# Kernel optimization log

Hardware: AMD Instinct MI355X
Metric: run time of the kernel (lower is better)

The kernel has to match this reference:

```python
import jax, jax.numpy as jnp
import numpy as np

NUM_TIMESCALES = 16
MAX_TIME = 100.0
N_HEADS = 4
MLP_WIDTH = 128
HIDDEN_EACH = 128  # hidden_size // attn_n_heads = 512 // 4


def setup_inputs() -> dict:
    key = jax.random.key(0)
    ks = jax.random.split(key, 8)
    B, ROWS_PER_PAT, V = 32, 64, 32
    R = B * ROWS_PER_PAT
    # patient i has counts[i] observations, laid out row-major in its block of rows
    counts = 512 + 16 * np.arange(B)
    M = np.zeros((R, V), np.int32)
    for i in range(B):
        flat = M[i * ROWS_PER_PAT:(i + 1) * ROWS_PER_PAT].reshape(-1)
        flat[:counts[i]] = 1
    n_obs = int(counts.sum())        # 24320
    max_n_obs = int(counts.max())    # 1008
    n_in = 2 * NUM_TIMESCALES + 2    # 34

    def lin(k, o, i_):
        kw, kb = jax.random.split(k)
        return (jax.random.normal(kw, (o, i_)) * (1.0 / np.sqrt(i_)),
                jax.random.normal(kb, (o,)) * 0.01)

    W0, b0 = lin(ks[0], MLP_WIDTH, n_in)
    W1, b1 = lin(ks[1], MLP_WIDTH, MLP_WIDTH)
    W2, b2 = lin(ks[2], HIDDEN_EACH, MLP_WIDTH)
    Wq, bq = lin(ks[3], HIDDEN_EACH, HIDDEN_EACH)
    Wk, bk = lin(ks[4], HIDDEN_EACH, HIDDEN_EACH)
    return {
        "times": jax.random.uniform(ks[5], (R,)) * MAX_TIME,
        "time_ptr": jnp.arange(R + 1),
        "X": jax.random.normal(ks[6], (R, V)),
        "M": jnp.asarray(M),
        "obs_idx": jnp.repeat(jnp.arange(B), ROWS_PER_PAT),
        "pat_idx": jnp.arange(B),
        "W0": W0, "b0": b0, "W1": W1, "b1": b1, "W2": W2, "b2": b2,
        "Wq": Wq, "bq": bq, "Wk": Wk, "bk": bk,
        "n_obs": n_obs, "max_n_obs": max_n_obs,
    }


def reference(times, time_ptr, X, M, obs_idx, pat_idx,
              W0, b0, W1, b1, W2, b2, Wq, bq, Wk, bk, n_obs, max_n_obs):
    B = pat_idx.shape[0]
    # --- ragged scatter: (time_row, var) observations -> padded per-patient sets ---
    rows, cols = jnp.nonzero(M, size=n_obs)          # row-major, grouped by patient
    p = obs_idx[rows]                                # patient id per observation
    vals = X[rows, cols]
    t_arr = jnp.repeat(times, jnp.diff(time_ptr), total_repeat_length=X.shape[0])
    t = t_arr[rows]
    lens = jnp.bincount(p, length=B)
    starts = jnp.cumsum(lens) - lens
    pos = jnp.arange(n_obs) - starts[p]              # within-patient slot index
    Sv = jnp.zeros((B, max_n_obs), X.dtype).at[p, pos].set(cols.astype(X.dtype))
    Sx = jnp.zeros((B, max_n_obs), X.dtype).at[p, pos].set(vals)
    St = jnp.zeros((B, max_n_obs), X.dtype).at[p, pos].set(t)
    pad = jnp.arange(max_n_obs)[None, :] >= lens[:, None]   # True = padding
    # --- time embedding + feature concat: [sin, cos, var, value] ---
    timescales = MAX_TIME ** jnp.linspace(0.0, 1.0, NUM_TIMESCALES)
    st = St[..., None] / timescales
    new_X = jnp.concatenate([jnp.sin(st), jnp.cos(st), Sv[..., None], Sx[..., None]], axis=-1)
    # --- encoder MLP (depth 3 -> 1 hidden layer, eval mode: dropout is identity) ---
    h = jax.nn.relu(new_X @ W0.T + b0)
    h = jax.nn.relu(h @ W1.T + b1)
    enc = h @ W2.T + b2                              # [B, L, 128]
    # --- masked self-attention weights (only q/k matter; output is discarded) ---
    L = max_n_obs
    hd = HIDDEN_EACH // N_HEADS
    q = (enc @ Wq.T + bq).reshape(B, L, N_HEADS, hd)
    k = (enc @ Wk.T + bk).reshape(B, L, N_HEADS, hd)
    scores = jnp.einsum('blhd,bmhd->bhlm', q, k) / np.sqrt(hd)
    scores = jnp.where(pad[:, None, None, :], -1e30, scores)
    attn = jax.nn.softmax(scores, axis=-1)           # [B, H, L, L]
    w = attn[:, :, -1, :]                            # last-query attention row
    summed = jnp.einsum('bhl,ble->bhe', w, enc)      # [B, H, 128]
    return summed.reshape(B, -1)                     # [B, 512]
```

## Files before the change

kernel.cpp:

```cpp
#include <hip/hip_runtime.h>

#define B_PAT 32
#define RTOT 2048
#define NV 32
#define LMAX 1008
#define NTS 16
#define NIN 64
#define TLD 72
#define HW 128
#define LDSP 136
#define NCH2 32
#define ELD 132
#define RLD 136

typedef __attribute__((ext_vector_type(8))) short short8;
typedef __attribute__((ext_vector_type(4))) float floatx4;

__device__ __forceinline__ ushort f2b(float f) {
  unsigned int x = __float_as_uint(f);
  unsigned int r = (x + 0x7FFFu + ((x >> 16) & 1u)) >> 16;
  return (ushort)r;
}
__device__ __forceinline__ unsigned int pack2(ushort lo, ushort hi) {
  return (unsigned int)lo | ((unsigned int)hi << 16);
}
__device__ __forceinline__ float tscale(int i) {
  return exp2f((float)i * (6.643856189774724f / 15.0f));
}

__global__ __launch_bounds__(256) void kA(
    const float* __restrict__ times, const int* __restrict__ time_ptr,
    const int* __restrict__ M, const float* __restrict__ W0,
    const float* __restrict__ W1, const float* __restrict__ W2,
    int* __restrict__ row_cnt, float* __restrict__ trow,
    ushort* __restrict__ W0p, ushort* __restrict__ W1b, ushort* __restrict__ W2b)
{
  const int blk = blockIdx.x, t = threadIdx.x;
  if (blk >= 8) {
    if (blk == 8) {
      for (int i = t; i < HW * NIN; i += 256) {
        int n = i >> 6, k = i & 63;
        W0p[i] = (k < 34) ? f2b(W0[n * 34 + k]) : (ushort)0;
      }
    } else if (blk == 9) {
      for (int i = t; i < HW * HW; i += 256) W1b[i] = f2b(W1[i]);
    } else {
      for (int i = t; i < HW * HW; i += 256) W2b[i] = f2b(W2[i]);
    }
    return;
  }
  const int r = blk * 256 + t;
  const int4* mp = (const int4*)(M + r * NV);
  int c = 0;
#pragma unroll
  for (int q = 0; q < 8; ++q) {
    int4 m4 = mp[q];
    c += (m4.x != 0) + (m4.y != 0) + (m4.z != 0) + (m4.w != 0);
  }
  row_cnt[r] = c;
  int lo = 0, hi = RTOT - 1;
  while (lo < hi) { int mid = (lo + hi + 1) >> 1; if (time_ptr[mid] <= r) lo = mid; else hi = mid - 1; }
  trow[r] = times[lo];
}

__global__ __launch_bounds__(256) void kB(
    const int* __restrict__ obs_idx, const int* __restrict__ row_cnt,
    int* __restrict__ base, int* __restrict__ rowstart, int* __restrict__ lens)
{
  const int t = threadIdx.x;
  const int lane = t & 63, wv = t >> 6;
  __shared__ int wsum[4];
  __shared__ int gpre[RTOT + 1];
  __shared__ int rowstart_s[B_PAT + 1];
  int cnt[8], pref[8];
  int a = 0;
  const int rbase = t * 8;
#pragma unroll
  for (int j = 0; j < 8; ++j) {
    cnt[j] = row_cnt[rbase + j];
    pref[j] = a; a += cnt[j];
  }
  int incl = a;
  for (int off = 1; off < 64; off <<= 1) {
    int v = __shfl_up(incl, off);
    if (lane >= off) incl += v;
  }
  if (lane == 63) wsum[wv] = incl;
  if (t == 0) rowstart_s[B_PAT] = RTOT;
  __syncthreads();
  int wbase = 0;
  for (int w = 0; w < wv; ++w) wbase += wsum[w];
  int excl = wbase + incl - a;
#pragma unroll
  for (int j = 0; j < 8; ++j) gpre[rbase + j] = excl + pref[j];
  if (t == 255) gpre[RTOT] = excl + a;
  for (int r = t; r < RTOT; r += 256) {
    int b = obs_idx[r];
    if (r == 0 || obs_idx[r - 1] != b) rowstart_s[b] = r;
  }
  __syncthreads();
  if (t < B_PAT) {
    int rs = rowstart_s[t], re = rowstart_s[t + 1];
    lens[t] = gpre[re] - gpre[rs];
    rowstart[t] = rs;
  }
  if (t == 0) rowstart[B_PAT] = RTOT;
  for (int r = t; r < RTOT; r += 256)
    base[r] = gpre[r] - gpre[rowstart_s[obs_idx[r]]];
}

__global__ __launch_bounds__(256) void kC(
    const int* __restrict__ M, const float* __restrict__ X,
    const float* __restrict__ trow, const int* __restrict__ base,
    const int* __restrict__ row_cnt, const int* __restrict__ rowstart,
    const int* __restrict__ lens,
    const float* __restrict__ W0, const float* __restrict__ b0,
    const float* __restrict__ W1, const float* __restrict__ b1,
    const float* __restrict__ W2, const float* __restrict__ b2,
    const float* __restrict__ Wq, const float* __restrict__ bq,
    const float* __restrict__ Wk, float* __restrict__ r_all)
{
  const int b = blockIdx.x;
  const int t = threadIdx.x;
  __shared__ float x_s[64];
  __shared__ float h0[HW], h1[HW], eq[HW], q_s[HW], part[256];
  __shared__ int rc_s[2];
  if (t < 64) x_s[t] = 0.0f;
  if (t == 0) {
    const int pos = LMAX - 1;
    if (pos < lens[b]) {
      int r = rowstart[b];
      while (base[r] + row_cnt[r] <= pos) ++r;
      int k = pos - base[r], c = 0;
      for (int cc = 0; cc < NV; ++cc)
        if (M[r * NV + cc] != 0) { if (k == 0) { c = cc; break; } --k; }
      rc_s[0] = r; rc_s[1] = c;
    } else rc_s[0] = -1;
  }
  __syncthreads();
  if (rc_s[0] < 0) {
    if (t >= 16 && t < 32) x_s[t] = 1.0f;
  } else {
    int r = rc_s[0], c = rc_s[1];
    if (t < 16) {
      float a = trow[r] / tscale(t);
      x_s[t] = sinf(a); x_s[16 + t] = cosf(a);
    }
    if (t == 0) { x_s[32] = (float)c; x_s[33] = X[r * NV + c]; }
  }
  __syncthreads();
  if (t < HW) {
    float a = b0[t];
#pragma unroll 2
    for (int k = 0; k < 34; ++k) a += W0[t * 34 + k] * x_s[k];
    h0[t] = fmaxf(a, 0.0f);
  }
  __syncthreads();
  {
    int oo = t & 127, hf = t >> 7;
    float a = 0.f;
    const float* wr = W1 + oo * HW + hf * 64;
#pragma unroll 8
    for (int k = 0; k < 64; ++k) a += wr[k] * h0[hf * 64 + k];
    part[t] = a;
  }
  __syncthreads();
  if (t < HW) h1[t] = fmaxf(part[t] + part[t + 128] + b1[t], 0.0f);
  __syncthreads();
  {
    int oo = t & 127, hf = t >> 7;
    float a = 0.f;
    const float* wr = W2 + oo * HW + hf * 64;
#pragma unroll 8
    for (int k = 0; k < 64; ++k) a += wr[k] * h1[hf * 64 + k];
    part[t] = a;
  }
  __syncthreads();
  if (t < HW) eq[t] = part[t] + part[t + 128] + b2[t];
  __syncthreads();
  {
    int oo = t & 127, hf = t >> 7;
    float a = 0.f;
    const float* wr = Wq + oo * HW + hf * 64;
#pragma unroll 8
    for (int k = 0; k < 64; ++k) a += wr[k] * eq[hf * 64 + k];
    part[t] = a;
  }
  __syncthreads();
  if (t < HW) q_s[t] = part[t] + part[t + 128] + bq[t];
  __syncthreads();
  const float scale = 0.17677669529663687f;
  for (int idx = t; idx < 512; idx += 256) {
    int h = idx >> 7, e = idx & 127;
    float a = 0.f;
#pragma unroll 8
    for (int d = 0; d < 32; ++d) a += Wk[(h * 32 + d) * HW + e] * q_s[h * 32 + d];
    r_all[b * 512 + idx] = a * scale;
  }
}

__global__ __launch_bounds__(256) void kD(
    const int* __restrict__ M, const float* __restrict__ X,
    const float* __restrict__ trow, const int* __restrict__ base,
    const int* __restrict__ row_cnt, const int* __restrict__ rowstart,
    const ushort* __restrict__ W0p, const float* __restrict__ b0,
    const ushort* __restrict__ W1b, const float* __restrict__ b1,
    const ushort* __restrict__ W2b, const float* __restrict__ b2,
    const float* __restrict__ r_all, float* __restrict__ partial,
    float2* __restrict__ mxsm)
{
  const int bx = blockIdx.x;
  const int b = bx >> 5, j = bx & 31;
  const int t = threadIdx.x;
  const int wv = t >> 6, lane = t & 63;
  const int rs = rowstart[b], re = rowstart[b + 1];
  const int r0 = rs + 2 * j;
  if (r0 >= re) {
    if (t < 4) mxsm[bx * 4 + t] = make_float2(-1e30f, 0.0f);
    return;
  }
  const int r1 = r0 + 1;
  const bool has1 = (r1 < re);
  const int pstart = base[r0];
  const int valid = row_cnt[r0] + (has1 ? row_cnt[r1] : 0);
  if (valid <= 0) {
    if (t < 4) mxsm[bx * 4 + t] = make_float2(-1e30f, 0.0f);
    return;
  }
  __shared__ __align__(16) char arena[55296];
  ushort* tile = (ushort*)(arena);
  ushort* bufA = (ushort*)(arena + 9216);
  float*  encs = (float*)(arena);
  ushort* bufB = (ushort*)(arena + 33792);
  float*  r_s  = (float*)(arena + 51200);
  float*  lg   = (float*)(arena + 53376);
  unsigned int* mapP = (unsigned int*)(arena + 54400);
  unsigned int* mapT = (unsigned int*)(arena + 54656);
  ushort* tps  = (ushort*)(arena + 54912);
  float*  mx_s = (float*)(arena + 55040);
  float*  sm_s = (float*)(arena + 55056);
  {
    uint4 z = make_uint4(0u, 0u, 0u, 0u);
    uint4* tp = (uint4*)tile;
    for (int i = t; i < 576; i += 256) tp[i] = z;
    for (int i = t; i < 512; i += 256)
      r_s[(i >> 7) * RLD + (i & 127)] = r_all[b * 512 + i];
  }
  __syncthreads();
  if (wv == 0) {
    int rr = lane >> 5, cc = lane & 31;
    int r = r0 + rr;
    bool present = (rr == 0 || has1) ? (M[r * NV + cc] != 0) : false;
    unsigned long long mask = __ballot(present);
    unsigned int mh = (rr == 0) ? (unsigned int)mask : (unsigned int)(mask >> 32);
    if (present) {
      int rank = __popc(mh & ((1u << cc) - 1u));
      int lp = base[r] - pstart + rank;
      mapP[lp] = pack2(f2b((float)cc), f2b(X[r * NV + cc]));
      mapT[lp] = (unsigned int)rr;
    }
  }
  if (wv == 1 && lane < 32) {
    int rr = lane >> 4, i = lane & 15;
    if (rr == 0 || has1) {
      float a = trow[r0 + rr] / tscale(i);
      tps[rr * 32 + i] = f2b(sinf(a));
      tps[rr * 32 + 16 + i] = f2b(cosf(a));
    }
  }
  __syncthreads();
  {
    int lp = t >> 2, jj = t & 3;
    if (lp < valid) {
      int rr = (int)mapT[lp];
      unsigned int* dst = (unsigned int*)(tile + lp * TLD);
      const unsigned int* tp = ((const unsigned int*)tps) + rr * 16;
      if (jj == 0) {
#pragma unroll
        for (int k = 0; k < 8; ++k) dst[k] = tp[k];
      } else if (jj == 1) {
#pragma unroll
        for (int k = 0; k < 8; ++k) dst[8 + k] = tp[8 + k];
      } else if (jj == 2) {
        dst[16] = mapP[lp];
      }
    }
  }
  __syncthreads();
  const int m16 = lane & 15, quad = lane >> 4;
  const int rowl = wv * 16 + m16;
  {
    const short8* ar = (const short8*)(tile + rowl * TLD);
    short8 a0 = ar[quad];
    short8 a1 = ar[4 + quad];
#pragma unroll
    for (int nt = 0; nt < 8; ++nt) {
      int n = nt * 16 + m16;
      const short8* br = (const short8*)(W0p + n * NIN);
      floatx4 acc = {0.f, 0.f, 0.f, 0.f};
      acc = __builtin_amdgcn_mfma_f32_16x16x32_bf16(a0, br[quad], acc, 0, 0, 0);
      acc = __builtin_amdgcn_mfma_f32_16x16x32_bf16(a1, br[4 + quad], acc, 0, 0, 0);
      float bias = b0[n];
#pragma unroll
      for (int i = 0; i < 4; ++i) {
        float vv = fmaxf(acc[i] + bias, 0.0f);
        bufA[(wv * 16 + quad * 4 + i) * LDSP + n] = f2b(vv);
      }
    }
  }
  __syncthreads();
  {
#pragma unroll
    for (int nt = 0; nt < 8; ++nt) {
      int n = nt * 16 + m16;
      floatx4 acc = {0.f, 0.f, 0.f, 0.f};
#pragma unroll
      for (int ks = 0; ks < 4; ++ks) {
        short8 a = *(const short8*)(bufA + rowl * LDSP + ks * 32 + quad * 8);
        short8 bb = *(const short8*)(W1b + n * HW + ks * 32 + quad * 8);
        acc = __builtin_amdgcn_mfma_f32_16x16x32_bf16(a, bb, acc, 0, 0, 0);
      }
      float bias = b1[n];
#pragma unroll
      for (int i = 0; i < 4; ++i) {
        float vv = fmaxf(acc[i] + bias, 0.0f);
        bufB[(wv * 16 + quad * 4 + i) * LDSP + n] = f2b(vv);
      }
    }
  }
  __syncthreads();
  {
#pragma unroll
    for (int nt = 0; nt < 8; ++nt) {
      int n = nt * 16 + m16;
      floatx4 acc = {0.f, 0.f, 0.f, 0.f};
#pragma unroll
      for (int ks = 0; ks < 4; ++ks) {
        short8 a = *(const short8*)(bufB + rowl * LDSP + ks * 32 + quad * 8);
        short8 bb = *(const short8*)(W2b + n * HW + ks * 32 + quad * 8);
        acc = __builtin_amdgcn_mfma_f32_16x16x32_bf16(a, bb, acc, 0, 0, 0);
      }
      float bias = b2[n];
#pragma unroll
      for (int i = 0; i < 4; ++i)
        encs[(wv * 16 + quad * 4 + i) * ELD + n] = acc[i] + bias;
    }
  }
  __syncthreads();
  {
    int m = t >> 2, h = t & 3;
    if (m < valid) {
      const float4* ev = (const float4*)(&encs[m * ELD]);
      const float4* rv = (const float4*)(&r_s[h * RLD]);
      float acc = 0.f;
#pragma unroll
      for (int e4 = 0; e4 < 32; ++e4) {
        float4 v = ev[e4], r = rv[e4];
        acc += v.x * r.x + v.y * r.y + v.z * r.z + v.w * r.w;
      }
      lg[h * 64 + m] = acc;
    }
  }
  __syncthreads();
  {
    float v = (lane < valid) ? lg[wv * 64 + lane] : -1e30f;
    float mx = v;
#pragma unroll
    for (int o = 32; o >= 1; o >>= 1) mx = fmaxf(mx, __shfl_xor(mx, o));
    float p = (lane < valid) ? expf(v - mx) : 0.f;
    lg[wv * 64 + lane] = p;
    float sm = p;
#pragma unroll
    for (int o = 32; o >= 1; o >>= 1) sm += __shfl_xor(sm, o);
    if (lane == 0) { mx_s[wv] = mx; sm_s[wv] = sm; }
  }
  __syncthreads();
  for (int idx = t; idx < 512; idx += 256) {
    int h = idx >> 7, e = idx & 127;
    float acc = 0.f;
    for (int m = 0; m < valid; ++m)
      acc += lg[h * 64 + m] * encs[m * ELD + e];
    partial[(size_t)bx * 512 + idx] = acc;
  }
  if (t < 4) mxsm[bx * 4 + t] = make_float2(mx_s[t], sm_s[t]);
}

__global__ __launch_bounds__(256) void k4_combine(
    const float* __restrict__ partial, const float2* __restrict__ mxsm,
    float* __restrict__ out)
{
  const int b = blockIdx.x;
  const int tid = threadIdx.x;
  __shared__ float f_s[NCH2 * 4];
  if (tid < 4) {
    int h = tid;
    float2 v[NCH2];
    float M = -1e30f;
#pragma unroll
    for (int c = 0; c < NCH2; ++c) {
      v[c] = mxsm[(b * NCH2 + c) * 4 + h];
      if (v[c].y > 0.f) M = fmaxf(M, v[c].x);
    }
    float S = 0.f;
#pragma unroll
    for (int c = 0; c < NCH2; ++c)
      if (v[c].y > 0.f) S += v[c].y * expf(v[c].x - M);
    float invS = 1.0f / S;
#pragma unroll
    for (int c = 0; c < NCH2; ++c)
      f_s[c * 4 + h] = (v[c].y > 0.f) ? expf(v[c].x - M) * invS : 0.f;
  }
  __syncthreads();
  for (int idx = tid; idx < 512; idx += 256) {
    int h = idx >> 7;
    float acc = 0.f;
#pragma unroll
    for (int c = 0; c < NCH2; ++c)
      acc += partial[((size_t)(b * NCH2 + c)) * 512 + idx] * f_s[c * 4 + h];
    out[b * 512 + idx] = acc;
  }
}

extern "C" void kernel_launch(void* const* d_in, const int* in_sizes, int n_in,
                              void* d_out, int out_size, void* d_ws, size_t ws_size,
                              hipStream_t stream) {
  const float* times = (const float*)d_in[0];
  const int* time_ptr = (const int*)d_in[1];
  const float* X = (const float*)d_in[2];
  const int* M = (const int*)d_in[3];
  const int* obs_idx = (const int*)d_in[4];
  const float* W0 = (const float*)d_in[6];
  const float* b0 = (const float*)d_in[7];
  const float* W1 = (const float*)d_in[8];
  const float* b1 = (const float*)d_in[9];
  const float* W2 = (const float*)d_in[10];
  const float* b2 = (const float*)d_in[11];
  const float* Wq = (const float*)d_in[12];
  const float* bq = (const float*)d_in[13];
  const float* Wk = (const float*)d_in[14];
  float* out = (float*)d_out;

  char* ws = (char*)d_ws;
  size_t off = 0;
  int* row_cnt = (int*)(ws + off); off += RTOT * 4;
  float* trow = (float*)(ws + off); off += RTOT * 4;
  int* base = (int*)(ws + off); off += RTOT * 4;
  int* rowstart = (int*)(ws + off); off += 256;
  int* lens = (int*)(ws + off); off += 256;
  ushort* W0p = (ushort*)(ws + off); off += (size_t)HW * NIN * 2;
  ushort* W1b = (ushort*)(ws + off); off += (size_t)HW * HW * 2;
  ushort* W2b = (ushort*)(ws + off); off += (size_t)HW * HW * 2;
  float* r_all = (float*)(ws + off); off += (size_t)B_PAT * 512 * 4;
  float* partial = (float*)(ws + off); off += (size_t)B_PAT * NCH2 * 512 * 4;
  float2* mxsm = (float2*)(ws + off); off += (size_t)B_PAT * NCH2 * 4 * 8;

  kA<<<11, 256, 0, stream>>>(times, time_ptr, M, W0, W1, W2, row_cnt, trow, W0p, W1b, W2b);
  kB<<<1, 256, 0, stream>>>(obs_idx, row_cnt, base, rowstart, lens);
  kC<<<B_PAT, 256, 0, stream>>>(M, X, trow, base, row_cnt, rowstart, lens,
                                W0, b0, W1, b1, W2, b2, Wq, bq, Wk, r_all);
  kD<<<B_PAT * NCH2, 256, 0, stream>>>(M, X, trow, base, row_cnt, rowstart,
                                       W0p, b0, W1b, b1, W2b, b2, r_all, partial, mxsm);
  k4_combine<<<B_PAT, 256, 0, stream>>>(partial, mxsm, out);
}
```

Measured before the change: 167.2 us.

## Fuse preprocessing kernels into per-patient prep and rechunk encoder by observation count

```diff
diff --git a/kernel.cpp b/kernel.cpp
--- a/kernel.cpp
+++ b/kernel.cpp
@@ -9,7 +9,8 @@
 #define TLD 72
 #define HW 128
 #define LDSP 136
-#define NCH2 32
+#define NCH 16
+#define CH 63
 #define ELD 132
 #define RLD 136
 
@@ -28,125 +29,102 @@
   return exp2f((float)i * (6.643856189774724f / 15.0f));
 }
 
-__global__ __launch_bounds__(256) void kA(
+__global__ __launch_bounds__(256) void kP(
     const float* __restrict__ times, const int* __restrict__ time_ptr,
-    const int* __restrict__ M, const float* __restrict__ W0,
-    const float* __restrict__ W1, const float* __restrict__ W2,
-    int* __restrict__ row_cnt, float* __restrict__ trow,
-    ushort* __restrict__ W0p, ushort* __restrict__ W1b, ushort* __restrict__ W2b)
-{
-  const int blk = blockIdx.x, t = threadIdx.x;
-  if (blk >= 8) {
-    if (blk == 8) {
-      for (int i = t; i < HW * NIN; i += 256) {
-        int n = i >> 6, k = i & 63;
-        W0p[i] = (k < 34) ? f2b(W0[n * 34 + k]) : (ushort)0;
-      }
-    } else if (blk == 9) {
-      for (int i = t; i < HW * HW; i += 256) W1b[i] = f2b(W1[i]);
-    } else {
-      for (int i = t; i < HW * HW; i += 256) W2b[i] = f2b(W2[i]);
-    }
-    return;
-  }
-  const int r = blk * 256 + t;
-  const int4* mp = (const int4*)(M + r * NV);
-  int c = 0;
-#pragma unroll
-  for (int q = 0; q < 8; ++q) {
-    int4 m4 = mp[q];
-    c += (m4.x != 0) + (m4.y != 0) + (m4.z != 0) + (m4.w != 0);
-  }
-  row_cnt[r] = c;
-  int lo = 0, hi = RTOT - 1;
-  while (lo < hi) { int mid = (lo + hi + 1) >> 1; if (time_ptr[mid] <= r) lo = mid; else hi = mid - 1; }
-  trow[r] = times[lo];
-}
-
-__global__ __launch_bounds__(256) void kB(
-    const int* __restrict__ obs_idx, const int* __restrict__ row_cnt,
-    int* __restrict__ base, int* __restrict__ rowstart, int* __restrict__ lens)
-{
-  const int t = threadIdx.x;
-  const int lane = t & 63, wv = t >> 6;
-  __shared__ int wsum[4];
-  __shared__ int gpre[RTOT + 1];
-  __shared__ int rowstart_s[B_PAT + 1];
-  int cnt[8], pref[8];
-  int a = 0;
-  const int rbase = t * 8;
-#pragma unroll
-  for (int j = 0; j < 8; ++j) {
-    cnt[j] = row_cnt[rbase + j];
-    pref[j] = a; a += cnt[j];
-  }
-  int incl = a;
-  for (int off = 1; off < 64; off <<= 1) {
-    int v = __shfl_up(incl, off);
-    if (lane >= off) incl += v;
-  }
-  if (lane == 63) wsum[wv] = incl;
-  if (t == 0) rowstart_s[B_PAT] = RTOT;
-  __syncthreads();
-  int wbase = 0;
-  for (int w = 0; w < wv; ++w) wbase += wsum[w];
-  int excl = wbase + incl - a;
-#pragma unroll
-  for (int j = 0; j < 8; ++j) gpre[rbase + j] = excl + pref[j];
-  if (t == 255) gpre[RTOT] = excl + a;
-  for (int r = t; r < RTOT; r += 256) {
-    int b = obs_idx[r];
-    if (r == 0 || obs_idx[r - 1] != b) rowstart_s[b] = r;
-  }
-  __syncthreads();
-  if (t < B_PAT) {
-    int rs = rowstart_s[t], re = rowstart_s[t + 1];
-    lens[t] = gpre[re] - gpre[rs];
-    rowstart[t] = rs;
-  }
-  if (t == 0) rowstart[B_PAT] = RTOT;
-  for (int r = t; r < RTOT; r += 256)
-    base[r] = gpre[r] - gpre[rowstart_s[obs_idx[r]]];
-}
-
-__global__ __launch_bounds__(256) void kC(
-    const int* __restrict__ M, const float* __restrict__ X,
-    const float* __restrict__ trow, const int* __restrict__ base,
-    const int* __restrict__ row_cnt, const int* __restrict__ rowstart,
-    const int* __restrict__ lens,
+    const float* __restrict__ X, const int* __restrict__ M,
+    const int* __restrict__ obs_idx,
     const float* __restrict__ W0, const float* __restrict__ b0,
     const float* __restrict__ W1, const float* __restrict__ b1,
     const float* __restrict__ W2, const float* __restrict__ b2,
     const float* __restrict__ Wq, const float* __restrict__ bq,
-    const float* __restrict__ Wk, float* __restrict__ r_all)
+    const float* __restrict__ Wk,
+    int* __restrict__ pbase_g, int* __restrict__ rowstart_g,
+    int* __restrict__ lens, float* __restrict__ trow_g,
+    ushort* __restrict__ W0p, ushort* __restrict__ W1b, ushort* __restrict__ W2b,
+    float* __restrict__ r_all)
 {
   const int b = blockIdx.x;
   const int t = threadIdx.x;
+  if (b >= B_PAT) {
+    if (b == B_PAT) {
+      for (int i = t; i < HW * NIN; i += 256) {
+        int n = i >> 6, k = i & 63;
+        W0p[i] = (k < 34) ? f2b(W0[n * 34 + k]) : (ushort)0;
+      }
+    } else if (b == B_PAT + 1) {
+      for (int i = t; i < HW * HW; i += 256) W1b[i] = f2b(W1[i]);
+    } else {
+      for (int i = t; i < HW * HW; i += 256) W2b[i] = f2b(W2[i]);
+    }
+    return;
+  }
+  __shared__ int rs_s, re_s;
+  __shared__ int cnt_s[64];
+  __shared__ int pbase_s[65];
+  __shared__ float tval_s[64];
+  __shared__ int qrc[3];
   __shared__ float x_s[64];
   __shared__ float h0[HW], h1[HW], eq[HW], q_s[HW], part[256];
-  __shared__ int rc_s[2];
+  for (int r = t * 8; r < t * 8 + 8; ++r) {
+    if (obs_idx[r] == b) {
+      if (r == 0 || obs_idx[r - 1] != b) rs_s = r;
+      if (r == RTOT - 1 || obs_idx[r + 1] != b) re_s = r + 1;
+    }
+  }
+  __syncthreads();
+  const int rs = rs_s, re = re_s;
+  const int n = re - rs;
+  if (t < 64) {
+    int c = 0;
+    if (t < n) {
+      const int4* mp = (const int4*)(M + (size_t)(rs + t) * NV);
+#pragma unroll
+      for (int q = 0; q < 8; ++q) {
+        int4 m4 = mp[q];
+        c += (m4.x != 0) + (m4.y != 0) + (m4.z != 0) + (m4.w != 0);
+      }
+      int lo = 0, hi = RTOT - 1, r = rs + t;
+      while (lo < hi) { int mid = (lo + hi + 1) >> 1; if (time_ptr[mid] <= r) lo = mid; else hi = mid - 1; }
+      tval_s[t] = times[lo];
+      trow_g[r] = times[lo];
+    }
+    cnt_s[t] = c;
+  }
+  __syncthreads();
+  if (t < 64) {
+    int incl = cnt_s[t];
+    for (int off = 1; off < 64; off <<= 1) {
+      int v = __shfl_up(incl, off);
+      if (t >= off) incl += v;
+    }
+    pbase_s[t + 1] = incl;
+    if (t == 0) pbase_s[0] = 0;
+  }
+  __syncthreads();
+  const int len = pbase_s[64];
+  if (t < 65) pbase_g[b * 65 + t] = pbase_s[t];
+  if (t == 0) { rowstart_g[b] = rs; lens[b] = len; }
+  if (t == 0) {
+    if (LMAX - 1 < len) {
+      int lr = 0;
+      while (pbase_s[lr + 1] <= LMAX - 1) ++lr;
+      int k = (LMAX - 1) - pbase_s[lr], col = 0;
+      for (int cc = 0; cc < NV; ++cc)
+        if (M[(size_t)(rs + lr) * NV + cc] != 0) { if (k == 0) { col = cc; break; } --k; }
+      qrc[0] = lr; qrc[1] = col; qrc[2] = 1;
+    } else qrc[2] = 0;
+  }
   if (t < 64) x_s[t] = 0.0f;
-  if (t == 0) {
-    const int pos = LMAX - 1;
-    if (pos < lens[b]) {
-      int r = rowstart[b];
-      while (base[r] + row_cnt[r] <= pos) ++r;
-      int k = pos - base[r], c = 0;
-      for (int cc = 0; cc < NV; ++cc)
-        if (M[r * NV + cc] != 0) { if (k == 0) { c = cc; break; } --k; }
-      rc_s[0] = r; rc_s[1] = c;
-    } else rc_s[0] = -1;
-  }
-  __syncthreads();
-  if (rc_s[0] < 0) {
+  __syncthreads();
+  if (qrc[2] == 0) {
     if (t >= 16 && t < 32) x_s[t] = 1.0f;
   } else {
-    int r = rc_s[0], c = rc_s[1];
+    int lr = qrc[0], col = qrc[1];
     if (t < 16) {
-      float a = trow[r] / tscale(t);
+      float a = tval_s[lr] / tscale(t);
       x_s[t] = sinf(a); x_s[16 + t] = cosf(a);
     }
-    if (t == 0) { x_s[32] = (float)c; x_s[33] = X[r * NV + c]; }
+    if (t == 0) { x_s[32] = (float)col; x_s[33] = X[(size_t)(rs + lr) * NV + col]; }
   }
   __syncthreads();
   if (t < HW) {
@@ -199,10 +177,10 @@
   }
 }
 
-__global__ __launch_bounds__(256) void kD(
+__global__ __launch_bounds__(256) void kF(
     const int* __restrict__ M, const float* __restrict__ X,
-    const float* __restrict__ trow, const int* __restrict__ base,
-    const int* __restrict__ row_cnt, const int* __restrict__ rowstart,
+    const int* __restrict__ pbase_g, const int* __restrict__ rowstart_g,
+    const int* __restrict__ lens, const float* __restrict__ trow_g,
     const ushort* __restrict__ W0p, const float* __restrict__ b0,
     const ushort* __restrict__ W1b, const float* __restrict__ b1,
     const ushort* __restrict__ W2b, const float* __restrict__ b2,
@@ -210,83 +188,76 @@
     float2* __restrict__ mxsm)
 {
   const int bx = blockIdx.x;
-  const int b = bx >> 5, j = bx & 31;
+  const int b = bx >> 4, c = bx & 15;
   const int t = threadIdx.x;
-  const int wv = t >> 6, lane = t & 63;
-  const int rs = rowstart[b], re = rowstart[b + 1];
-  const int r0 = rs + 2 * j;
-  if (r0 >= re) {
-    if (t < 4) mxsm[bx * 4 + t] = make_float2(-1e30f, 0.0f);
-    return;
-  }
-  const int r1 = r0 + 1;
-  const bool has1 = (r1 < re);
-  const int pstart = base[r0];
-  const int valid = row_cnt[r0] + (has1 ? row_cnt[r1] : 0);
+  const int len = lens[b];
+  const int start = c * CH;
+  int valid = len - start; if (valid > CH) valid = CH;
   if (valid <= 0) {
     if (t < 4) mxsm[bx * 4 + t] = make_float2(-1e30f, 0.0f);
     return;
   }
-  __shared__ __align__(16) char arena[55296];
-  ushort* tile = (ushort*)(arena);
-  ushort* bufA = (ushort*)(arena + 9216);
-  float*  encs = (float*)(arena);
-  ushort* bufB = (ushort*)(arena + 33792);
-  float*  r_s  = (float*)(arena + 51200);
-  float*  lg   = (float*)(arena + 53376);
-  unsigned int* mapP = (unsigned int*)(arena + 54400);
-  unsigned int* mapT = (unsigned int*)(arena + 54656);
-  ushort* tps  = (ushort*)(arena + 54912);
-  float*  mx_s = (float*)(arena + 55040);
-  float*  sm_s = (float*)(arena + 55056);
+  __shared__ ushort tile[64 * TLD];
+  __shared__ ushort bufA[64 * LDSP];
+  __shared__ ushort bufB[64 * LDSP];
+  __shared__ float encs[64 * ELD];
+  __shared__ float r_s[4 * RLD];
+  __shared__ float lg[4 * 64];
+  __shared__ unsigned int umask[64];
+  __shared__ float tval[64];
+  __shared__ int pbase_s[65];
+  __shared__ float inv_ts[NTS];
+  __shared__ float mx_s[4], sm_s[4];
+  const int rs = rowstart_g[b];
   {
     uint4 z = make_uint4(0u, 0u, 0u, 0u);
     uint4* tp = (uint4*)tile;
-    for (int i = t; i < 576; i += 256) tp[i] = z;
+    for (int i = t; i < 64 * TLD / 8; i += 256) tp[i] = z;
     for (int i = t; i < 512; i += 256)
       r_s[(i >> 7) * RLD + (i & 127)] = r_all[b * 512 + i];
   }
-  __syncthreads();
-  if (wv == 0) {
-    int rr = lane >> 5, cc = lane & 31;
-    int r = r0 + rr;
-    bool present = (rr == 0 || has1) ? (M[r * NV + cc] != 0) : false;
-    unsigned long long mask = __ballot(present);
-    unsigned int mh = (rr == 0) ? (unsigned int)mask : (unsigned int)(mask >> 32);
-    if (present) {
-      int rank = __popc(mh & ((1u << cc) - 1u));
-      int lp = base[r] - pstart + rank;
-      mapP[lp] = pack2(f2b((float)cc), f2b(X[r * NV + cc]));
-      mapT[lp] = (unsigned int)rr;
-    }
-  }
-  if (wv == 1 && lane < 32) {
-    int rr = lane >> 4, i = lane & 15;
-    if (rr == 0 || has1) {
-      float a = trow[r0 + rr] / tscale(i);
-      tps[rr * 32 + i] = f2b(sinf(a));
-      tps[rr * 32 + 16 + i] = f2b(cosf(a));
-    }
-  }
-  __syncthreads();
-  {
-    int lp = t >> 2, jj = t & 3;
-    if (lp < valid) {
-      int rr = (int)mapT[lp];
-      unsigned int* dst = (unsigned int*)(tile + lp * TLD);
-      const unsigned int* tp = ((const unsigned int*)tps) + rr * 16;
-      if (jj == 0) {
-#pragma unroll
-        for (int k = 0; k < 8; ++k) dst[k] = tp[k];
-      } else if (jj == 1) {
-#pragma unroll
-        for (int k = 0; k < 8; ++k) dst[8 + k] = tp[8 + k];
-      } else if (jj == 2) {
-        dst[16] = mapP[lp];
-      }
-    }
-  }
-  __syncthreads();
+  if (t < 64) {
+    int r = rs + t;
+    unsigned int mk = 0;
+    const int* mp = M + (size_t)r * NV;
+#pragma unroll
+    for (int cc = 0; cc < NV; ++cc) mk |= (mp[cc] != 0 ? 1u : 0u) << cc;
+    umask[t] = mk;
+    tval[t] = trow_g[r];
+  } else if (t < 129) {
+    pbase_s[t - 64] = pbase_g[b * 65 + (t - 64)];
+  } else if (t >= 136 && t < 136 + NTS) {
+    inv_ts[t - 136] = 1.0f / tscale(t - 136);
+  }
+  __syncthreads();
+  {
+    int pos = t >> 2, sub = t & 3;
+    if (pos < valid) {
+      int gpos = start + pos;
+      int lo = 0, hi = 63;
+      while (lo < hi) { int mid = (lo + hi + 1) >> 1; if (pbase_s[mid] <= gpos) lo = mid; else hi = mid - 1; }
+      int lrow = lo;
+      int rank = gpos - pbase_s[lrow];
+      unsigned int m = umask[lrow];
+      for (int i = 0; i < rank; ++i) m &= m - 1;
+      int col = (m != 0u) ? __builtin_ctz(m) : 0;
+      float tv = tval[lrow];
+      unsigned int* dst = (unsigned int*)(tile + pos * TLD);
+      if (sub == 0) {
+#pragma unroll
+        for (int w = 0; w < 8; ++w)
+          dst[w] = pack2(f2b(sinf(tv * inv_ts[2 * w])), f2b(sinf(tv * inv_ts[2 * w + 1])));
+      } else if (sub == 1) {
+#pragma unroll
+        for (int w = 0; w < 8; ++w)
+          dst[8 + w] = pack2(f2b(cosf(tv * inv_ts[2 * w])), f2b(cosf(tv * inv_ts[2 * w + 1])));
+      } else if (sub == 2) {
+        dst[16] = pack2(f2b((float)col), f2b(X[(size_t)(rs + lrow) * NV + col]));
+      }
+    }
+  }
+  __syncthreads();
+  const int wv = t >> 6, lane = t & 63;
   const int m16 = lane & 15, quad = lane >> 4;
   const int rowl = wv * 16 + m16;
   {
@@ -295,16 +266,16 @@
     short8 a1 = ar[4 + quad];
 #pragma unroll
     for (int nt = 0; nt < 8; ++nt) {
-      int n = nt * 16 + m16;
-      const short8* br = (const short8*)(W0p + n * NIN);
+      int nn = nt * 16 + m16;
+      const short8* br = (const short8*)(W0p + nn * NIN);
       floatx4 acc = {0.f, 0.f, 0.f, 0.f};
       acc = __builtin_amdgcn_mfma_f32_16x16x32_bf16(a0, br[quad], acc, 0, 0, 0);
       acc = __builtin_amdgcn_mfma_f32_16x16x32_bf16(a1, br[4 + quad], acc, 0, 0, 0);
-      float bias = b0[n];
+      float bias = b0[nn];
 #pragma unroll
       for (int i = 0; i < 4; ++i) {
         float vv = fmaxf(acc[i] + bias, 0.0f);
-        bufA[(wv * 16 + quad * 4 + i) * LDSP + n] = f2b(vv);
+        bufA[(wv * 16 + quad * 4 + i) * LDSP + nn] = f2b(vv);
       }
     }
   }
@@ -312,19 +283,19 @@
   {
 #pragma unroll
     for (int nt = 0; nt < 8; ++nt) {
-      int n = nt * 16 + m16;
+      int nn = nt * 16 + m16;
       floatx4 acc = {0.f, 0.f, 0.f, 0.f};
 #pragma unroll
       for (int ks = 0; ks < 4; ++ks) {
         short8 a = *(const short8*)(bufA + rowl * LDSP + ks * 32 + quad * 8);
-        short8 bb = *(const short8*)(W1b + n * HW + ks * 32 + quad * 8);
+        short8 bb = *(const short8*)(W1b + nn * HW + ks * 32 + quad * 8);
         acc = __builtin_amdgcn_mfma_f32_16x16x32_bf16(a, bb, acc, 0, 0, 0);
       }
-      float bias = b1[n];
+      float bias = b1[nn];
 #pragma unroll
       for (int i = 0; i < 4; ++i) {
         float vv = fmaxf(acc[i] + bias, 0.0f);
-        bufB[(wv * 16 + quad * 4 + i) * LDSP + n] = f2b(vv);
+        bufB[(wv * 16 + quad * 4 + i) * LDSP + nn] = f2b(vv);
       }
     }
   }
@@ -332,18 +303,18 @@
   {
 #pragma unroll
     for (int nt = 0; nt < 8; ++nt) {
-      int n = nt * 16 + m16;
+      int nn = nt * 16 + m16;
       floatx4 acc = {0.f, 0.f, 0.f, 0.f};
 #pragma unroll
       for (int ks = 0; ks < 4; ++ks) {
         short8 a = *(const short8*)(bufB + rowl * LDSP + ks * 32 + quad * 8);
-        short8 bb = *(const short8*)(W2b + n * HW + ks * 32 + quad * 8);
+        short8 bb = *(const short8*)(W2b + nn * HW + ks * 32 + quad * 8);
         acc = __builtin_amdgcn_mfma_f32_16x16x32_bf16(a, bb, acc, 0, 0, 0);
       }
-      float bias = b2[n];
+      float bias = b2[nn];
 #pragma unroll
       for (int i = 0; i < 4; ++i)
-        encs[(wv * 16 + quad * 4 + i) * ELD + n] = acc[i] + bias;
+        encs[(wv * 16 + quad * 4 + i) * ELD + nn] = acc[i] + bias;
     }
   }
   __syncthreads();
@@ -385,29 +356,29 @@
   if (t < 4) mxsm[bx * 4 + t] = make_float2(mx_s[t], sm_s[t]);
 }
 
-__global__ __launch_bounds__(256) void k4_combine(
+__global__ __launch_bounds__(256) void kK(
     const float* __restrict__ partial, const float2* __restrict__ mxsm,
     float* __restrict__ out)
 {
   const int b = blockIdx.x;
   const int tid = threadIdx.x;
-  __shared__ float f_s[NCH2 * 4];
+  __shared__ float f_s[NCH * 4];
   if (tid < 4) {
     int h = tid;
-    float2 v[NCH2];
+    float2 v[NCH];
     float M = -1e30f;
 #pragma unroll
-    for (int c = 0; c < NCH2; ++c) {
-      v[c] = mxsm[(b * NCH2 + c) * 4 + h];
+    for (int c = 0; c < NCH; ++c) {
+      v[c] = mxsm[(b * NCH + c) * 4 + h];
       if (v[c].y > 0.f) M = fmaxf(M, v[c].x);
     }
     float S = 0.f;
 #pragma unroll
-    for (int c = 0; c < NCH2; ++c)
+    for (int c = 0; c < NCH; ++c)
       if (v[c].y > 0.f) S += v[c].y * expf(v[c].x - M);
     float invS = 1.0f / S;
 #pragma unroll
-    for (int c = 0; c < NCH2; ++c)
+    for (int c = 0; c < NCH; ++c)
       f_s[c * 4 + h] = (v[c].y > 0.f) ? expf(v[c].x - M) * invS : 0.f;
   }
   __syncthreads();
@@ -415,8 +386,10 @@
     int h = idx >> 7;
     float acc = 0.f;
 #pragma unroll
-    for (int c = 0; c < NCH2; ++c)
-      acc += partial[((size_t)(b * NCH2 + c)) * 512 + idx] * f_s[c * 4 + h];
+    for (int c = 0; c < NCH; ++c) {
+      float f = f_s[c * 4 + h];
+      if (f > 0.f) acc += partial[((size_t)(b * NCH + c)) * 512 + idx] * f;
+    }
     out[b * 512 + idx] = acc;
   }
 }
@@ -442,23 +415,23 @@
 
   char* ws = (char*)d_ws;
   size_t off = 0;
-  int* row_cnt = (int*)(ws + off); off += RTOT * 4;
-  float* trow = (float*)(ws + off); off += RTOT * 4;
-  int* base = (int*)(ws + off); off += RTOT * 4;
-  int* rowstart = (int*)(ws + off); off += 256;
+  int* pbase_g = (int*)(ws + off); off += (size_t)B_PAT * 65 * 4;
+  int* rowstart_g = (int*)(ws + off); off += 256;
   int* lens = (int*)(ws + off); off += 256;
+  float* trow_g = (float*)(ws + off); off += RTOT * 4;
   ushort* W0p = (ushort*)(ws + off); off += (size_t)HW * NIN * 2;
   ushort* W1b = (ushort*)(ws + off); off += (size_t)HW * HW * 2;
   ushort* W2b = (ushort*)(ws + off); off += (size_t)HW * HW * 2;
   float* r_all = (float*)(ws + off); off += (size_t)B_PAT * 512 * 4;
-  float* partial = (float*)(ws + off); off += (size_t)B_PAT * NCH2 * 512 * 4;
-  float2* mxsm = (float2*)(ws + off); off += (size_t)B_PAT * NCH2 * 4 * 8;
-
-  kA<<<11, 256, 0, stream>>>(times, time_ptr, M, W0, W1, W2, row_cnt, trow, W0p, W1b, W2b);
-  kB<<<1, 256, 0, stream>>>(obs_idx, row_cnt, base, rowstart, lens);
-  kC<<<B_PAT, 256, 0, stream>>>(M, X, trow, base, row_cnt, rowstart, lens,
-                                W0, b0, W1, b1, W2, b2, Wq, bq, Wk, r_all);
-  kD<<<B_PAT * NCH2, 256, 0, stream>>>(M, X, trow, base, row_cnt, rowstart,
-                                       W0p, b0, W1b, b1, W2b, b2, r_all, partial, mxsm);
-  k4_combine<<<B_PAT, 256, 0, stream>>>(partial, mxsm, out);
-}
+  float* partial = (float*)(ws + off); off += (size_t)B_PAT * NCH * 512 * 4;
+  float2* mxsm = (float2*)(ws + off); off += (size_t)B_PAT * NCH * 4 * 8;
+
+  kP<<<B_PAT + 3, 256, 0, stream>>>(times, time_ptr, X, M, obs_idx,
+                                    W0, b0, W1, b1, W2, b2, Wq, bq, Wk,
+                                    pbase_g, rowstart_g, lens, trow_g,
+                                    W0p, W1b, W2b, r_all);
+  kF<<<B_PAT * NCH, 256, 0, stream>>>(M, X, pbase_g, rowstart_g, lens, trow_g,
+                                      W0p, b0, W1b, b1, W2b, b2, r_all,
+                                      partial, mxsm);
+  kK<<<B_PAT, 256, 0, stream>>>(partial, mxsm, out);
+}
```

Result: faster. 147.2 us (-12.0%).
